# Kernel tuning notes

Hardware: AMD Instinct MI355X
Metric: run time of the kernel (lower is better)

Reference implementation:

```python
import jax, jax.numpy as jnp
import numpy as np

TEMP = 0.3
LAM = 0.9
NUM_LABELS = 7
B, D = 8192, 768


def setup_inputs() -> dict:
    key = jax.random.key(0)
    k1, k2, k3, k4 = jax.random.split(key, 4)
    cls_emb = jax.random.normal(k1, (B, D), dtype=jnp.float32)
    pooled = jax.random.normal(k2, (B, D), dtype=jnp.float32)
    labels = jax.random.randint(k3, (B,), 0, NUM_LABELS)
    W = jax.random.normal(k4, (NUM_LABELS, D), dtype=jnp.float32) * 0.02
    b = jnp.zeros((NUM_LABELS,), dtype=jnp.float32)
    return {"cls_emb": cls_emb, "pooled": pooled, "labels": labels, "W": W, "b": b}


def reference(cls_emb, pooled, labels, W, b):
    # classifier head (dropout = identity in eval)
    logits = pooled @ W.T + b  # [B, num_labels]

    # cross-entropy (mean reduction, as nn.CrossEntropyLoss default)
    logp = jax.nn.log_softmax(logits, axis=-1)
    ce = -jnp.mean(jnp.take_along_axis(logp, labels[:, None], axis=1)[:, 0])

    # supervised contrastive loss on DETACHED cls embeddings (original uses .detach().numpy())
    e = jax.lax.stop_gradient(cls_emb)
    en = e / jnp.linalg.norm(e, axis=1, keepdims=True)
    S = (en @ en.T) / TEMP  # [B, B] scaled cosine similarity
    n = S.shape[0]
    eye = jnp.eye(n, dtype=bool)
    # row_sum excludes the diagonal -> stable off-diagonal logsumexp
    lse = jax.nn.logsumexp(jnp.where(eye, -jnp.inf, S), axis=1)  # [B]
    pos = (labels[:, None] == labels[None, :]) & ~eye  # [B, B]
    n_i = jnp.sum(pos, axis=1).astype(S.dtype)  # positives per anchor
    inner = jnp.sum(jnp.where(pos, S - lse[:, None], 0.0), axis=1)  # sum log(exp(s)/row_sum)
    per_anchor = jnp.where(n_i > 0, -inner / jnp.maximum(n_i, 1.0), 0.0)
    contrastive = jnp.sum(per_anchor)  # summed over anchors, as in original

    loss = LAM * contrastive + (1.0 - LAM) * ce
    return loss, logits
```

## Files before the change

kernel.cpp:

```cpp
#include <hip/hip_runtime.h>
#include <hip/hip_bf16.h>


#define B_N 8192
#define D_K 768
#define NLAB 7
#define MBOUND 3.3333333333333335f
#define RTINV 1.8257418583505538f

typedef short s16x8 __attribute__((ext_vector_type(8)));
typedef float f32x4 __attribute__((ext_vector_type(4)));

__device__ __forceinline__ void gl2lds16(const void* g, void* l) {
  __builtin_amdgcn_global_load_lds(
      (const __attribute__((address_space(1))) void*)g,
      (__attribute__((address_space(3))) void*)l, 16, 0, 0);
}

__device__ __forceinline__ float bf16u_to_f(unsigned short u) {
  unsigned int w = ((unsigned int)u) << 16;
  return __uint_as_float(w);
}

__global__ __launch_bounds__(256) void k_norm(const float* __restrict__ cls,
                                              unsigned short* __restrict__ en) {
  int row = blockIdx.x * 4 + (threadIdx.x >> 6);
  int lane = threadIdx.x & 63;
  const float4* src = (const float4*)(cls + (size_t)row * D_K);
  float4 x[3];
  float ss = 0.f;
#pragma unroll
  for (int j = 0; j < 3; ++j) {
    x[j] = src[j * 64 + lane];
    ss += x[j].x * x[j].x + x[j].y * x[j].y + x[j].z * x[j].z + x[j].w * x[j].w;
  }
#pragma unroll
  for (int m = 1; m < 64; m <<= 1) ss += __shfl_xor(ss, m);
  float sc = rsqrtf(ss) * RTINV;
  ushort4* dst = (ushort4*)(en + (size_t)row * D_K);
#pragma unroll
  for (int j = 0; j < 3; ++j) {
    const float* xv = reinterpret_cast<const float*>(&x[j]);
    ushort4 o;
    unsigned short* ov = reinterpret_cast<unsigned short*>(&o);
#pragma unroll
    for (int k = 0; k < 4; ++k) {
      __hip_bfloat16 h = __float2bfloat16(xv[k] * sc);
      ov[k] = *reinterpret_cast<unsigned short*>(&h);
    }
    dst[j * 64 + lane] = o;
  }
}

__global__ __launch_bounds__(256) void k_hist(const int* __restrict__ labels,
                                              int* __restrict__ hist) {
  int cnt[NLAB];
#pragma unroll
  for (int c = 0; c < NLAB; ++c) cnt[c] = 0;
  int base = blockIdx.x * 1024 + threadIdx.x;
#pragma unroll
  for (int j = 0; j < 4; ++j) {
    int lab = labels[base + j * 256];
#pragma unroll
    for (int c = 0; c < NLAB; ++c) cnt[c] += (lab == c);
  }
#pragma unroll
  for (int c = 0; c < NLAB; ++c)
#pragma unroll
    for (int m = 1; m < 64; m <<= 1) cnt[c] += __shfl_xor(cnt[c], m);
  if ((threadIdx.x & 63) == 0)
#pragma unroll
    for (int c = 0; c < NLAB; ++c) atomicAdd(&hist[c], cnt[c]);
}

__global__ __launch_bounds__(192) void k_classumA(const unsigned short* __restrict__ en,
                                                  const int* __restrict__ labels,
                                                  float* __restrict__ partial) {
  int g = blockIdx.x, t = threadIdx.x;
  float acc[NLAB][4];
#pragma unroll
  for (int c = 0; c < NLAB; ++c)
#pragma unroll
    for (int k = 0; k < 4; ++k) acc[c][k] = 0.f;
  int r0 = g * 128;
  for (int r = 0; r < 128; r += 4) {
    int lab[4];
    ushort4 u[4];
#pragma unroll
    for (int q = 0; q < 4; ++q) {
      int row = r0 + r + q;
      lab[q] = labels[row];
      u[q] = *(const ushort4*)(en + (size_t)row * D_K + t * 4);
    }
#pragma unroll
    for (int q = 0; q < 4; ++q) {
      float x0 = bf16u_to_f(u[q].x), x1 = bf16u_to_f(u[q].y);
      float x2 = bf16u_to_f(u[q].z), x3 = bf16u_to_f(u[q].w);
#pragma unroll
      for (int c = 0; c < NLAB; ++c) {
        bool m = (lab[q] == c);
        acc[c][0] += m ? x0 : 0.f;
        acc[c][1] += m ? x1 : 0.f;
        acc[c][2] += m ? x2 : 0.f;
        acc[c][3] += m ? x3 : 0.f;
      }
    }
  }
  float* dst = partial + (size_t)g * (NLAB * D_K);
#pragma unroll
  for (int c = 0; c < NLAB; ++c) {
    float4 v = {acc[c][0], acc[c][1], acc[c][2], acc[c][3]};
    *(float4*)(dst + c * D_K + t * 4) = v;
  }
}

__global__ __launch_bounds__(256) void k_classumB(const float* __restrict__ partial,
                                                  float* __restrict__ T) {
  int idx = blockIdx.x * 256 + threadIdx.x;
  float v = 0.f;
  for (int g = 0; g < 64; ++g) v += partial[(size_t)g * (NLAB * D_K) + idx];
  T[idx] = v;
}

__global__ __launch_bounds__(256) void k_classum_atomic(
    const unsigned short* __restrict__ en, const int* __restrict__ labels,
    float* __restrict__ T) {
  int g = blockIdx.x / 3;
  int kk = (blockIdx.x % 3) * 256 + threadIdx.x;
  float acc[NLAB];
#pragma unroll
  for (int c = 0; c < NLAB; ++c) acc[c] = 0.f;
  int r0 = g * 512;
  for (int r = 0; r < 512; ++r) {
    int row = r0 + r;
    int lab = labels[row];
    float x = bf16u_to_f(en[(size_t)row * D_K + kk]);
#pragma unroll
    for (int c = 0; c < NLAB; ++c) acc[c] += (lab == c) ? x : 0.f;
  }
#pragma unroll
  for (int c = 0; c < NLAB; ++c) atomicAdd(&T[c * D_K + kk], acc[c]);
}

__global__ __launch_bounds__(256) void k_logits_ce(
    const float* __restrict__ pooled, const int* __restrict__ labels,
    const float* __restrict__ W, const float* __restrict__ bias,
    float* __restrict__ logits_out, float* __restrict__ celoss) {
  int row = blockIdx.x * 4 + (threadIdx.x >> 6);
  int lane = threadIdx.x & 63;
  const float4* p4 = (const float4*)(pooled + (size_t)row * D_K);
  float acc[NLAB];
#pragma unroll
  for (int c = 0; c < NLAB; ++c) acc[c] = 0.f;
#pragma unroll
  for (int j = 0; j < 3; ++j) {
    float4 x = p4[j * 64 + lane];
#pragma unroll
    for (int c = 0; c < NLAB; ++c) {
      float4 w = ((const float4*)(W + c * D_K))[j * 64 + lane];
      acc[c] += x.x * w.x + x.y * w.y + x.z * w.z + x.w * w.w;
    }
  }
#pragma unroll
  for (int c = 0; c < NLAB; ++c)
#pragma unroll
    for (int m = 1; m < 64; m <<= 1) acc[c] += __shfl_xor(acc[c], m);
  if (lane == 0) {
    float l[NLAB], mx = -1e30f;
#pragma unroll
    for (int c = 0; c < NLAB; ++c) { l[c] = acc[c] + bias[c]; mx = fmaxf(mx, l[c]); }
    float se = 0.f;
#pragma unroll
    for (int c = 0; c < NLAB; ++c) se += __expf(l[c] - mx);
    float lse = mx + __logf(se);
    celoss[row] = lse - l[labels[row]];
    float* o = logits_out + (size_t)row * NLAB;
#pragma unroll
    for (int c = 0; c < NLAB; ++c) o[c] = l[c];
  }
}

__global__ __launch_bounds__(256) void k_scl(const unsigned short* __restrict__ en,
                                             float* __restrict__ rse) {
  __shared__ __align__(16) unsigned short As[128 * 64];
  __shared__ __align__(16) unsigned short Bs[128 * 64];

  int rem = blockIdx.x;
  int BI = 0, BJ = 0;
  for (;;) {
    int sz = (BI == BJ) ? 36 : 64;
    if (rem < sz) break;
    rem -= sz;
    if (++BJ == 8) { ++BI; BJ = BI; }
  }
  int bi, bj;
  if (BI == BJ) {
    int r = 0, w = 8;
    while (rem >= w) { rem -= w; ++r; --w; }
    bi = BI * 8 + r;
    bj = BJ * 8 + r + rem;
  } else {
    bi = BI * 8 + (rem >> 3);
    bj = BJ * 8 + (rem & 7);
  }

  const int i0 = bi * 128, j0 = bj * 128;
  const int tid = threadIdx.x, wv = tid >> 6, lane = tid & 63;
  const int quad = lane >> 4, cix = lane & 15;
  const int rowTile = 64 * (wv >> 1), colTile = 64 * (wv & 1);

  f32x4 acc[4][4] = {};

  for (int kc = 0; kc < 12; ++kc) {
    __syncthreads();
#pragma unroll
    for (int it = 0; it < 4; ++it) {
      int s = it * 256 + tid;
      int r = s >> 3;
      int c = ((s & 7) - r) & 7;
      int lbase = (it * 256 + wv * 64) * 16;
      gl2lds16(en + (size_t)(i0 + r) * D_K + kc * 64 + c * 8, (char*)As + lbase);
      gl2lds16(en + (size_t)(j0 + r) * D_K + kc * 64 + c * 8, (char*)Bs + lbase);
    }
    __syncthreads();
#pragma unroll
    for (int h = 0; h < 2; ++h) {
      const int cc = quad + 4 * h;
      s16x8 aF[4];
#pragma unroll
      for (int mt = 0; mt < 4; ++mt) {
        int r = rowTile + 16 * mt + cix;
        aF[mt] = *reinterpret_cast<const s16x8*>((const char*)As +
                                                 (r * 8 + ((cc + r) & 7)) * 16);
      }
#pragma unroll
      for (int nt = 0; nt < 4; ++nt) {
        int r = colTile + 16 * nt + cix;
        s16x8 bF = *reinterpret_cast<const s16x8*>((const char*)Bs +
                                                   (r * 8 + ((cc + r) & 7)) * 16);
#pragma unroll
        for (int mt = 0; mt < 4; ++mt)
          acc[mt][nt] = __builtin_amdgcn_mfma_f32_16x16x32_bf16(
              aF[mt], bF, acc[mt][nt], 0, 0, 0);
      }
    }
  }

  if (bi != bj) {
    float ce_col[4] = {0.f, 0.f, 0.f, 0.f};
#pragma unroll
    for (int mt = 0; mt < 4; ++mt) {
      int rowbase = i0 + rowTile + 16 * mt + quad * 4;
      float rs_e[4] = {0.f, 0.f, 0.f, 0.f};
#pragma unroll
      for (int nt = 0; nt < 4; ++nt) {
#pragma unroll
        for (int rg = 0; rg < 4; ++rg) {
          float e = __expf(acc[mt][nt][rg] - MBOUND);
          rs_e[rg] += e;
          ce_col[nt] += e;
        }
      }
#pragma unroll
      for (int rg = 0; rg < 4; ++rg)
#pragma unroll
        for (int m = 1; m <= 8; m <<= 1) rs_e[rg] += __shfl_xor(rs_e[rg], m);
      if (cix == 0)
#pragma unroll
        for (int rg = 0; rg < 4; ++rg) atomicAdd(&rse[rowbase + rg], rs_e[rg]);
    }
#pragma unroll
    for (int nt = 0; nt < 4; ++nt) {
      ce_col[nt] += __shfl_xor(ce_col[nt], 16);
      ce_col[nt] += __shfl_xor(ce_col[nt], 32);
    }
    if (quad == 0)
#pragma unroll
      for (int nt = 0; nt < 4; ++nt)
        atomicAdd(&rse[j0 + colTile + 16 * nt + cix], ce_col[nt]);
  } else {
#pragma unroll
    for (int mt = 0; mt < 4; ++mt) {
      int rowbase = i0 + rowTile + 16 * mt + quad * 4;
      float rs_e[4] = {0.f, 0.f, 0.f, 0.f};
#pragma unroll
      for (int nt = 0; nt < 4; ++nt) {
        int gcol = j0 + colTile + 16 * nt + cix;
#pragma unroll
        for (int rg = 0; rg < 4; ++rg) {
          bool dg = (rowbase + rg) == gcol;
          rs_e[rg] += dg ? 0.f : __expf(acc[mt][nt][rg] - MBOUND);
        }
      }
#pragma unroll
      for (int rg = 0; rg < 4; ++rg)
#pragma unroll
        for (int m = 1; m <= 8; m <<= 1) rs_e[rg] += __shfl_xor(rs_e[rg], m);
      if (cix == 0)
#pragma unroll
        for (int rg = 0; rg < 4; ++rg) atomicAdd(&rse[rowbase + rg], rs_e[rg]);
    }
  }
}

__global__ __launch_bounds__(256) void k_rowfinal(const float* __restrict__ rse,
                                                  const unsigned short* __restrict__ en,
                                                  const float* __restrict__ T,
                                                  const int* __restrict__ labels,
                                                  const int* __restrict__ hist,
                                                  const float* __restrict__ celoss,
                                                  float* __restrict__ contrP) {
  __shared__ float part[4];
  int wv = threadIdx.x >> 6, lane = threadIdx.x & 63;
  int row = blockIdx.x * 4 + wv;
  int l = labels[row];
  const ushort4* e4 = (const ushort4*)(en + (size_t)row * D_K);
  const float4* t4 = (const float4*)(T + (size_t)l * D_K);
  float pd = 0.f, sd = 0.f;
#pragma unroll
  for (int j = 0; j < 3; ++j) {
    ushort4 u = e4[j * 64 + lane];
    float4 t = t4[j * 64 + lane];
    float a0 = bf16u_to_f(u.x), a1 = bf16u_to_f(u.y);
    float a2 = bf16u_to_f(u.z), a3 = bf16u_to_f(u.w);
    pd += a0 * t.x + a1 * t.y + a2 * t.z + a3 * t.w;
    sd += a0 * a0 + a1 * a1 + a2 * a2 + a3 * a3;
  }
#pragma unroll
  for (int m = 1; m < 64; m <<= 1) {
    pd += __shfl_xor(pd, m);
    sd += __shfl_xor(sd, m);
  }
  if (lane == 0) {
    int ni = hist[l] - 1;
    float per = 0.f;
    if (ni > 0) {
      float possum = pd - sd;
      per = MBOUND + __logf(rse[row]) - possum / (float)ni;
    }
    part[wv] = 0.9f * per + (0.1f / (float)B_N) * celoss[row];
  }
  __syncthreads();
  if (threadIdx.x == 0) {
    float v = part[0] + part[1] + part[2] + part[3];
    atomicAdd(&contrP[(blockIdx.x & 63) * 16], v);
  }
}

__global__ void k_final(const float* __restrict__ contrP, float* __restrict__ out) {
  float v = contrP[threadIdx.x * 16];
#pragma unroll
  for (int m = 1; m < 64; m <<= 1) v += __shfl_xor(v, m);
  if (threadIdx.x == 0) out[0] = v;
}

extern "C" void kernel_launch(void* const* d_in, const int* in_sizes, int n_in,
                              void* d_out, int out_size, void* d_ws, size_t ws_size,
                              hipStream_t stream) {
  const float* cls    = (const float*)d_in[0];
  const float* pooled = (const float*)d_in[1];
  const int*   labels = (const int*)d_in[2];
  const float* W      = (const float*)d_in[3];
  const float* bias   = (const float*)d_in[4];
  float* out = (float*)d_out;

  char* ws = (char*)d_ws;
  unsigned short* en = (unsigned short*)ws;
  size_t off = (size_t)B_N * D_K * 2;
  float* rse     = (float*)(ws + off);
  int*   hist    = (int*)(ws + off + 32768);
  float* contrP  = (float*)(ws + off + 36864);
  float* celoss  = (float*)(ws + off + 40960);
  float* T       = (float*)(ws + off + 73728);
  float* partial = (float*)(ws + off + 98304);
  size_t need_partial = off + 98304 + 64 * (size_t)(NLAB * D_K) * 4;
  bool big_ws = ws_size >= need_partial;

  hipMemsetAsync(ws + off, 0, big_ws ? 40960 : 98304, stream);

  k_norm<<<B_N / 4, 256, 0, stream>>>(cls, en);
  k_hist<<<8, 256, 0, stream>>>(labels, hist);
  if (big_ws) {
    k_classumA<<<64, 192, 0, stream>>>(en, labels, partial);
    k_classumB<<<21, 256, 0, stream>>>(partial, T);
  } else {
    k_classum_atomic<<<48, 256, 0, stream>>>(en, labels, T);
  }
  k_logits_ce<<<B_N / 4, 256, 0, stream>>>(pooled, labels, W, bias, out + 1, celoss);
  k_scl<<<2080, 256, 0, stream>>>(en, rse);
  k_rowfinal<<<B_N / 4, 256, 0, stream>>>(rse, en, T, labels, hist, celoss, contrP);
  k_final<<<1, 64, 0, stream>>>(contrP, out);
}
```

Before: 243.9 us.

## Fuse prep kernels, fold histogram into classum, and finalize via last-block reduction

Merges normalization and logits/CE into one k_prep kernel and moves workspace zeroing into block 0 of that kernel, replacing the memset. The label histogram now runs in an extra wavefront of k_classumA, and the final reduction is done by the last-finishing block of k_rowfinal through a done counter, which removes k_final. The goal is fewer launches and less launch overhead. The risk is that block 0 zeroes rse while other k_prep blocks run, but nothing in k_prep reads rse, so later kernels see zeroed buffers.

```diff
diff --git a/kernel.cpp b/kernel.cpp
--- a/kernel.cpp
+++ b/kernel.cpp
@@ -22,10 +22,18 @@
   return __uint_as_float(w);
 }
 
-__global__ __launch_bounds__(256) void k_norm(const float* __restrict__ cls,
-                                              unsigned short* __restrict__ en) {
-  int row = blockIdx.x * 4 + (threadIdx.x >> 6);
-  int lane = threadIdx.x & 63;
+__global__ __launch_bounds__(256) void k_prep(
+    const float* __restrict__ cls, const float* __restrict__ pooled,
+    const int* __restrict__ labels, const float* __restrict__ W,
+    const float* __restrict__ bias, unsigned short* __restrict__ en,
+    float* __restrict__ logits_out, float* __restrict__ celoss,
+    int* __restrict__ zr) {
+  if (blockIdx.x == 0)
+    for (int t = threadIdx.x; t < 9280; t += 256) zr[t] = 0;
+
+  int wv = threadIdx.x >> 6, lane = threadIdx.x & 63;
+  int row = blockIdx.x * 4 + wv;
+
   const float4* src = (const float4*)(cls + (size_t)row * D_K);
   float4 x[3];
   float ss = 0.f;
@@ -50,67 +58,98 @@
     }
     dst[j * 64 + lane] = o;
   }
-}
-
-__global__ __launch_bounds__(256) void k_hist(const int* __restrict__ labels,
-                                              int* __restrict__ hist) {
-  int cnt[NLAB];
-#pragma unroll
-  for (int c = 0; c < NLAB; ++c) cnt[c] = 0;
-  int base = blockIdx.x * 1024 + threadIdx.x;
-#pragma unroll
-  for (int j = 0; j < 4; ++j) {
-    int lab = labels[base + j * 256];
-#pragma unroll
-    for (int c = 0; c < NLAB; ++c) cnt[c] += (lab == c);
+
+  const float4* p4 = (const float4*)(pooled + (size_t)row * D_K);
+  float acc[NLAB];
+#pragma unroll
+  for (int c = 0; c < NLAB; ++c) acc[c] = 0.f;
+#pragma unroll
+  for (int j = 0; j < 3; ++j) {
+    float4 xx = p4[j * 64 + lane];
+#pragma unroll
+    for (int c = 0; c < NLAB; ++c) {
+      float4 w = ((const float4*)(W + c * D_K))[j * 64 + lane];
+      acc[c] += xx.x * w.x + xx.y * w.y + xx.z * w.z + xx.w * w.w;
+    }
   }
 #pragma unroll
   for (int c = 0; c < NLAB; ++c)
 #pragma unroll
-    for (int m = 1; m < 64; m <<= 1) cnt[c] += __shfl_xor(cnt[c], m);
-  if ((threadIdx.x & 63) == 0)
-#pragma unroll
-    for (int c = 0; c < NLAB; ++c) atomicAdd(&hist[c], cnt[c]);
-}
-
-__global__ __launch_bounds__(192) void k_classumA(const unsigned short* __restrict__ en,
+    for (int m = 1; m < 64; m <<= 1) acc[c] += __shfl_xor(acc[c], m);
+  if (lane == 0) {
+    float l[NLAB], mx = -1e30f;
+#pragma unroll
+    for (int c = 0; c < NLAB; ++c) { l[c] = acc[c] + bias[c]; mx = fmaxf(mx, l[c]); }
+    float se = 0.f;
+#pragma unroll
+    for (int c = 0; c < NLAB; ++c) se += __expf(l[c] - mx);
+    float lse = mx + __logf(se);
+    celoss[row] = lse - l[labels[row]];
+    float* o = logits_out + (size_t)row * NLAB;
+#pragma unroll
+    for (int c = 0; c < NLAB; ++c) o[c] = l[c];
+  }
+}
+
+__global__ __launch_bounds__(256) void k_classumA(const unsigned short* __restrict__ en,
                                                   const int* __restrict__ labels,
-                                                  float* __restrict__ partial) {
+                                                  float* __restrict__ partial,
+                                                  int* __restrict__ hist) {
   int g = blockIdx.x, t = threadIdx.x;
-  float acc[NLAB][4];
-#pragma unroll
-  for (int c = 0; c < NLAB; ++c)
-#pragma unroll
-    for (int k = 0; k < 4; ++k) acc[c][k] = 0.f;
   int r0 = g * 128;
-  for (int r = 0; r < 128; r += 4) {
-    int lab[4];
-    ushort4 u[4];
-#pragma unroll
-    for (int q = 0; q < 4; ++q) {
-      int row = r0 + r + q;
-      lab[q] = labels[row];
-      u[q] = *(const ushort4*)(en + (size_t)row * D_K + t * 4);
-    }
-#pragma unroll
-    for (int q = 0; q < 4; ++q) {
-      float x0 = bf16u_to_f(u[q].x), x1 = bf16u_to_f(u[q].y);
-      float x2 = bf16u_to_f(u[q].z), x3 = bf16u_to_f(u[q].w);
-#pragma unroll
-      for (int c = 0; c < NLAB; ++c) {
-        bool m = (lab[q] == c);
-        acc[c][0] += m ? x0 : 0.f;
-        acc[c][1] += m ? x1 : 0.f;
-        acc[c][2] += m ? x2 : 0.f;
-        acc[c][3] += m ? x3 : 0.f;
-      }
-    }
-  }
-  float* dst = partial + (size_t)g * (NLAB * D_K);
-#pragma unroll
-  for (int c = 0; c < NLAB; ++c) {
-    float4 v = {acc[c][0], acc[c][1], acc[c][2], acc[c][3]};
-    *(float4*)(dst + c * D_K + t * 4) = v;
+  if (t < 192) {
+    float acc[NLAB][4];
+#pragma unroll
+    for (int c = 0; c < NLAB; ++c)
+#pragma unroll
+      for (int k = 0; k < 4; ++k) acc[c][k] = 0.f;
+    for (int r = 0; r < 128; r += 4) {
+      int lab[4];
+      ushort4 u[4];
+#pragma unroll
+      for (int q = 0; q < 4; ++q) {
+        int row = r0 + r + q;
+        lab[q] = labels[row];
+        u[q] = *(const ushort4*)(en + (size_t)row * D_K + t * 4);
+      }
+#pragma unroll
+      for (int q = 0; q < 4; ++q) {
+        float x0 = bf16u_to_f(u[q].x), x1 = bf16u_to_f(u[q].y);
+        float x2 = bf16u_to_f(u[q].z), x3 = bf16u_to_f(u[q].w);
+#pragma unroll
+        for (int c = 0; c < NLAB; ++c) {
+          bool m = (lab[q] == c);
+          acc[c][0] += m ? x0 : 0.f;
+          acc[c][1] += m ? x1 : 0.f;
+          acc[c][2] += m ? x2 : 0.f;
+          acc[c][3] += m ? x3 : 0.f;
+        }
+      }
+    }
+    float* dst = partial + (size_t)g * (NLAB * D_K);
+#pragma unroll
+    for (int c = 0; c < NLAB; ++c) {
+      float4 v = {acc[c][0], acc[c][1], acc[c][2], acc[c][3]};
+      *(float4*)(dst + c * D_K + t * 4) = v;
+    }
+  } else {
+    int lane = t - 192;
+    int cnt[NLAB];
+#pragma unroll
+    for (int c = 0; c < NLAB; ++c) cnt[c] = 0;
+#pragma unroll
+    for (int q = 0; q < 2; ++q) {
+      int lab = labels[r0 + q * 64 + lane];
+#pragma unroll
+      for (int c = 0; c < NLAB; ++c) cnt[c] += (lab == c);
+    }
+#pragma unroll
+    for (int c = 0; c < NLAB; ++c)
+#pragma unroll
+      for (int m = 1; m < 64; m <<= 1) cnt[c] += __shfl_xor(cnt[c], m);
+    if (lane == 0)
+#pragma unroll
+      for (int c = 0; c < NLAB; ++c) atomicAdd(&hist[c], cnt[c]);
   }
 }
 
@@ -120,64 +159,6 @@
   float v = 0.f;
   for (int g = 0; g < 64; ++g) v += partial[(size_t)g * (NLAB * D_K) + idx];
   T[idx] = v;
-}
-
-__global__ __launch_bounds__(256) void k_classum_atomic(
-    const unsigned short* __restrict__ en, const int* __restrict__ labels,
-    float* __restrict__ T) {
-  int g = blockIdx.x / 3;
-  int kk = (blockIdx.x % 3) * 256 + threadIdx.x;
-  float acc[NLAB];
-#pragma unroll
-  for (int c = 0; c < NLAB; ++c) acc[c] = 0.f;
-  int r0 = g * 512;
-  for (int r = 0; r < 512; ++r) {
-    int row = r0 + r;
-    int lab = labels[row];
-    float x = bf16u_to_f(en[(size_t)row * D_K + kk]);
-#pragma unroll
-    for (int c = 0; c < NLAB; ++c) acc[c] += (lab == c) ? x : 0.f;
-  }
-#pragma unroll
-  for (int c = 0; c < NLAB; ++c) atomicAdd(&T[c * D_K + kk], acc[c]);
-}
-
-__global__ __launch_bounds__(256) void k_logits_ce(
-    const float* __restrict__ pooled, const int* __restrict__ labels,
-    const float* __restrict__ W, const float* __restrict__ bias,
-    float* __restrict__ logits_out, float* __restrict__ celoss) {
-  int row = blockIdx.x * 4 + (threadIdx.x >> 6);
-  int lane = threadIdx.x & 63;
-  const float4* p4 = (const float4*)(pooled + (size_t)row * D_K);
-  float acc[NLAB];
-#pragma unroll
-  for (int c = 0; c < NLAB; ++c) acc[c] = 0.f;
-#pragma unroll
-  for (int j = 0; j < 3; ++j) {
-    float4 x = p4[j * 64 + lane];
-#pragma unroll
-    for (int c = 0; c < NLAB; ++c) {
-      float4 w = ((const float4*)(W + c * D_K))[j * 64 + lane];
-      acc[c] += x.x * w.x + x.y * w.y + x.z * w.z + x.w * w.w;
-    }
-  }
-#pragma unroll
-  for (int c = 0; c < NLAB; ++c)
-#pragma unroll
-    for (int m = 1; m < 64; m <<= 1) acc[c] += __shfl_xor(acc[c], m);
-  if (lane == 0) {
-    float l[NLAB], mx = -1e30f;
-#pragma unroll
-    for (int c = 0; c < NLAB; ++c) { l[c] = acc[c] + bias[c]; mx = fmaxf(mx, l[c]); }
-    float se = 0.f;
-#pragma unroll
-    for (int c = 0; c < NLAB; ++c) se += __expf(l[c] - mx);
-    float lse = mx + __logf(se);
-    celoss[row] = lse - l[labels[row]];
-    float* o = logits_out + (size_t)row * NLAB;
-#pragma unroll
-    for (int c = 0; c < NLAB; ++c) o[c] = l[c];
-  }
 }
 
 __global__ __launch_bounds__(256) void k_scl(const unsigned short* __restrict__ en,
@@ -303,13 +284,12 @@
   }
 }
 
-__global__ __launch_bounds__(256) void k_rowfinal(const float* __restrict__ rse,
-                                                  const unsigned short* __restrict__ en,
-                                                  const float* __restrict__ T,
-                                                  const int* __restrict__ labels,
-                                                  const int* __restrict__ hist,
-                                                  const float* __restrict__ celoss,
-                                                  float* __restrict__ contrP) {
+__global__ __launch_bounds__(256) void k_rowfinal(
+    const float* __restrict__ rse, const unsigned short* __restrict__ en,
+    const float* __restrict__ T, const int* __restrict__ labels,
+    const int* __restrict__ hist, const float* __restrict__ celoss,
+    float* __restrict__ contrP, int* __restrict__ done_count,
+    float* __restrict__ out) {
   __shared__ float part[4];
   int wv = threadIdx.x >> 6, lane = threadIdx.x & 63;
   int row = blockIdx.x * 4 + wv;
@@ -344,14 +324,16 @@
   if (threadIdx.x == 0) {
     float v = part[0] + part[1] + part[2] + part[3];
     atomicAdd(&contrP[(blockIdx.x & 63) * 16], v);
-  }
-}
-
-__global__ void k_final(const float* __restrict__ contrP, float* __restrict__ out) {
-  float v = contrP[threadIdx.x * 16];
-#pragma unroll
-  for (int m = 1; m < 64; m <<= 1) v += __shfl_xor(v, m);
-  if (threadIdx.x == 0) out[0] = v;
+    __threadfence();
+    int n = atomicAdd(done_count, 1);
+    if (n == (int)gridDim.x - 1) {
+      float s = 0.f;
+      for (int i = 0; i < 64; ++i)
+        s += __hip_atomic_load(&contrP[i * 16], __ATOMIC_RELAXED,
+                               __HIP_MEMORY_SCOPE_AGENT);
+      out[0] = s;
+    }
+  }
 }
 
 extern "C" void kernel_launch(void* const* d_in, const int* in_sizes, int n_in,
@@ -369,25 +351,18 @@
   size_t off = (size_t)B_N * D_K * 2;
   float* rse     = (float*)(ws + off);
   int*   hist    = (int*)(ws + off + 32768);
-  float* contrP  = (float*)(ws + off + 36864);
-  float* celoss  = (float*)(ws + off + 40960);
-  float* T       = (float*)(ws + off + 73728);
+  int*   done    = (int*)(ws + off + 32896);
+  float* contrP  = (float*)(ws + off + 33024);
+  float* T       = (float*)(ws + off + 37120);
+  float* celoss  = (float*)(ws + off + 58624);
   float* partial = (float*)(ws + off + 98304);
-  size_t need_partial = off + 98304 + 64 * (size_t)(NLAB * D_K) * 4;
-  bool big_ws = ws_size >= need_partial;
-
-  hipMemsetAsync(ws + off, 0, big_ws ? 40960 : 98304, stream);
-
-  k_norm<<<B_N / 4, 256, 0, stream>>>(cls, en);
-  k_hist<<<8, 256, 0, stream>>>(labels, hist);
-  if (big_ws) {
-    k_classumA<<<64, 192, 0, stream>>>(en, labels, partial);
-    k_classumB<<<21, 256, 0, stream>>>(partial, T);
-  } else {
-    k_classum_atomic<<<48, 256, 0, stream>>>(en, labels, T);
-  }
-  k_logits_ce<<<B_N / 4, 256, 0, stream>>>(pooled, labels, W, bias, out + 1, celoss);
+  int*   zr      = (int*)(ws + off);
+
+  k_prep<<<B_N / 4, 256, 0, stream>>>(cls, pooled, labels, W, bias, en, out + 1,
+                                      celoss, zr);
+  k_classumA<<<64, 256, 0, stream>>>(en, labels, partial, hist);
+  k_classumB<<<21, 256, 0, stream>>>(partial, T);
   k_scl<<<2080, 256, 0, stream>>>(en, rse);
-  k_rowfinal<<<B_N / 4, 256, 0, stream>>>(rse, en, T, labels, hist, celoss, contrP);
-  k_final<<<1, 64, 0, stream>>>(contrP, out);
-}
+  k_rowfinal<<<B_N / 4, 256, 0, stream>>>(rse, en, T, labels, hist, celoss, contrP,
+                                          done, out);
+}
```

New measurement: 272.9 us. 1.12x slower.
